# Kernel optimization log

Hardware: AMD Instinct MI355X
Metric: run time of the kernel (lower is better)

Reference implementation:

```python
import jax, jax.numpy as jnp
import numpy as np

N = 100000   # nodes
E = 1600000  # edges per meta-path graph
D_IN = 256
H = 4        # num_heads
F = 32       # out_feats per head
D_HID = H * F  # 128
D_SEM = 128  # semantic attention hidden dim
C = 8        # output classes
NEG_SLOPE = 0.2


def setup_inputs() -> dict:
    key = jax.random.key(0)
    ks = jax.random.split(key, 24)
    inp = {
        "x": jax.random.normal(ks[0], (N, D_IN), dtype=jnp.float32),
        "src0": jax.random.randint(ks[1], (E,), 0, N),
        "dst0": jax.random.randint(ks[2], (E,), 0, N),
        "ew0": jax.random.uniform(ks[3], (E,), dtype=jnp.float32),
        "src1": jax.random.randint(ks[4], (E,), 0, N),
        "dst1": jax.random.randint(ks[5], (E,), 0, N),
        "ew1": jax.random.uniform(ks[6], (E,), dtype=jnp.float32),
    }
    s_in = 1.0 / np.sqrt(D_IN)
    s_f = 1.0 / np.sqrt(F)
    s_h = 1.0 / np.sqrt(D_HID)
    s_s = 1.0 / np.sqrt(D_SEM)
    # GAT params for meta-path 0 and 1 (tuple feat -> separate fc_src/fc_dst)
    inp["Wsrc0"] = jax.random.normal(ks[7], (D_IN, D_HID), dtype=jnp.float32) * s_in
    inp["Wdst0"] = jax.random.normal(ks[8], (D_IN, D_HID), dtype=jnp.float32) * s_in
    inp["al0"] = jax.random.normal(ks[9], (H, F), dtype=jnp.float32) * s_f
    inp["ar0"] = jax.random.normal(ks[10], (H, F), dtype=jnp.float32) * s_f
    inp["b0"] = jnp.zeros((D_HID,), dtype=jnp.float32)
    inp["Wsrc1"] = jax.random.normal(ks[11], (D_IN, D_HID), dtype=jnp.float32) * s_in
    inp["Wdst1"] = jax.random.normal(ks[12], (D_IN, D_HID), dtype=jnp.float32) * s_in
    inp["al1"] = jax.random.normal(ks[13], (H, F), dtype=jnp.float32) * s_f
    inp["ar1"] = jax.random.normal(ks[14], (H, F), dtype=jnp.float32) * s_f
    inp["b1"] = jnp.zeros((D_HID,), dtype=jnp.float32)
    # Semantic attention: Linear(D_HID->128) -> tanh -> Linear(128->1, no bias)
    inp["Wp1"] = jax.random.normal(ks[15], (D_HID, D_SEM), dtype=jnp.float32) * s_h
    inp["bp1"] = jnp.zeros((D_SEM,), dtype=jnp.float32)
    inp["Wp2"] = jax.random.normal(ks[16], (D_SEM, 1), dtype=jnp.float32) * s_s
    # Prediction head
    inp["Wo"] = jax.random.normal(ks[17], (D_HID, C), dtype=jnp.float32) * s_h
    inp["bo"] = jnp.zeros((C,), dtype=jnp.float32)
    return inp


def gat_conv(x, Wsrc, Wdst, al, ar, b, src, dst, ew):
    # feat_src/feat_dst: [N, H, F]
    fs = (x @ Wsrc).reshape(N, H, F)
    fd = (x @ Wdst).reshape(N, H, F)
    el = jnp.einsum('nhf,hf->nh', fs, al)  # [N, H]
    er = jnp.einsum('nhf,hf->nh', fd, ar)  # [N, H]
    e = jax.nn.leaky_relu(el[src] + er[dst], negative_slope=NEG_SLOPE)  # [E, H]
    a = jax.nn.sigmoid(e) * ew[:, None]  # [E, H]  (sigmoid attention * edge_weight)
    m = fs[src] * a[:, :, None]  # [E, H, F]
    out = jax.ops.segment_sum(m, dst, num_segments=N)  # [N, H, F]
    out = out + b.reshape(1, H, F)
    return jax.nn.elu(out).reshape(N, H * F)


def semantic_attention(z, Wp1, bp1, Wp2):
    # z: [N, P, D_HID]
    w = jnp.tanh(z @ Wp1 + bp1) @ Wp2  # [N, P, 1]
    w = w.mean(axis=0)                  # [P, 1]
    beta = jax.nn.softmax(w, axis=0)    # softmax over meta-paths
    return (beta[None] * z).sum(axis=1)  # [N, D_HID]


def reference(x, src0, dst0, ew0, src1, dst1, ew1,
              Wsrc0, Wdst0, al0, ar0, b0,
              Wsrc1, Wdst1, al1, ar1, b1,
              Wp1, bp1, Wp2, Wo, bo):
    z0 = gat_conv(x, Wsrc0, Wdst0, al0, ar0, b0, src0, dst0, ew0)
    z1 = gat_conv(x, Wsrc1, Wdst1, al1, ar1, b1, src1, dst1, ew1)
    z = jnp.stack([z0, z1], axis=1)  # [N, 2, H*F]
    h = semantic_attention(z, Wp1, bp1, Wp2)  # [N, H*F]
    return h @ Wo + bo  # [N, C]
```

## Files before the change

kernel.cpp:

```cpp
#include <hip/hip_runtime.h>
#include <hip/hip_fp16.h>
#include <math.h>

#define N_NODES 100000
#define N_EDGES 1600000
#define D_IN    256
#define D_HID   128
#define NH      4
#define NF      32
#define D_SEM   128
#define NC      8
#define NEG_SLOPE 0.2f
#define BUCKET  64
#define BIN_SHIFT 9
#define BINS    196
#define BIN_CAP 9216
#define CHUNK   8192

typedef _Float16 half8 __attribute__((ext_vector_type(8)));
typedef float    floatx4 __attribute__((ext_vector_type(4)));

__global__ void prep_fold(const float* __restrict__ Ws0, const float* __restrict__ al0,
                          const float* __restrict__ Wd0, const float* __restrict__ ar0,
                          const float* __restrict__ Ws1, const float* __restrict__ al1,
                          const float* __restrict__ Wd1, const float* __restrict__ ar1,
                          float* __restrict__ WF) {
    int d = threadIdx.x;
    for (int p = 0; p < 2; ++p) {
        const float* Ws = p ? Ws1 : Ws0;
        const float* al = p ? al1 : al0;
        const float* Wd = p ? Wd1 : Wd0;
        const float* ar = p ? ar1 : ar0;
        for (int h = 0; h < NH; ++h) {
            float se = 0.f, sr = 0.f;
            for (int f = 0; f < NF; ++f) {
                se = fmaf(Ws[d*D_HID + h*NF + f], al[h*NF + f], se);
                sr = fmaf(Wd[d*D_HID + h*NF + f], ar[h*NF + f], sr);
            }
            WF[d*16 + p*8 + h]     = se;
            WF[d*16 + p*8 + 4 + h] = sr;
        }
    }
}

__global__ __launch_bounds__(256) void prep_tr(const float* __restrict__ Ws0,
                                               const float* __restrict__ Ws1,
                                               const float* __restrict__ Wp1,
                                               __half* __restrict__ WT0,
                                               __half* __restrict__ WT1,
                                               __half* __restrict__ WP1T) {
    int g = blockIdx.x * 256 + threadIdx.x;
    if (g < 32768) {
        int c = g >> 8, k = g & 255;
        WT0[g] = __float2half_rn(Ws0[k*D_HID + c]);
    } else if (g < 65536) {
        int g2 = g - 32768;
        int c = g2 >> 8, k = g2 & 255;
        WT1[g2] = __float2half_rn(Ws1[k*D_HID + c]);
    } else {
        int g2 = g - 65536;
        int c = g2 >> 7, k = g2 & 127;
        WP1T[g2] = __float2half_rn(Wp1[k*D_SEM + c]);
    }
}

__global__ __launch_bounds__(256) void er_el_kernel(const float* __restrict__ x,
                                                    const float* __restrict__ WF,
                                                    float* __restrict__ eler) {
    __shared__ float xs[16][260];
    __shared__ float wfs[4096];
    int tid = threadIdx.x;
    #pragma unroll
    for (int i = 0; i < 16; ++i) wfs[tid + i*256] = WF[tid + i*256];
    int n0 = blockIdx.x * 16;
    #pragma unroll
    for (int i = 0; i < 4; ++i) {
        int id = tid + i*256;
        int r = id >> 6, c = (id & 63) << 2;
        *(float4*)&xs[r][c] = *(const float4*)&x[(size_t)(n0 + r)*D_IN + c];
    }
    __syncthreads();
    int node = tid >> 4, c = tid & 15;
    float s = 0.f;
    #pragma unroll 8
    for (int k = 0; k < 256; ++k) s = fmaf(xs[node][k], wfs[k*16 + c], s);
    int p = c >> 3, e = (c >> 2) & 1, h = c & 3;
    eler[(p*2 + e)*400000 + (n0 + node)*4 + h] = s;
}

__global__ __launch_bounds__(256) void gemm_fs_mfma(const float* __restrict__ x,
                                                    const __half* __restrict__ WT,
                                                    __half* __restrict__ FS) {
    __shared__ unsigned short xs[64][64];
    __shared__ unsigned short ws[128][64];
    int tid = threadIdx.x;
    int row0 = blockIdx.x * 64;
    int wid = tid >> 6, lane = tid & 63;
    int wm = wid >> 1, wn = wid & 1;
    int lr = lane & 15, lk = lane >> 4;

    floatx4 acc[2][4];
    #pragma unroll
    for (int m = 0; m < 2; ++m)
        #pragma unroll
        for (int n = 0; n < 4; ++n) acc[m][n] = (floatx4){0.f, 0.f, 0.f, 0.f};

    for (int k0 = 0; k0 < D_IN; k0 += 64) {
        #pragma unroll
        for (int i = 0; i < 4; ++i) {
            int id = tid + i*256;
            int r = id >> 4, c4 = (id & 15) << 2;
            int grow = row0 + r;
            float4 v = make_float4(0.f, 0.f, 0.f, 0.f);
            if (grow < N_NODES) v = *(const float4*)&x[(size_t)grow*D_IN + k0 + c4];
            __half2 p0 = __floats2half2_rn(v.x, v.y);
            __half2 p1 = __floats2half2_rn(v.z, v.w);
            uint2 pk; pk.x = *(unsigned*)&p0; pk.y = *(unsigned*)&p1;
            int cc = (((c4 >> 3) ^ (r & 7)) << 3) + (c4 & 7);
            *(uint2*)&xs[r][cc] = pk;
        }
        #pragma unroll
        for (int i = 0; i < 8; ++i) {
            int id = tid + i*256;
            int col = id >> 4, c4 = (id & 15) << 2;
            uint2 pk = *(const uint2*)&WT[col*256 + k0 + c4];
            int cc = (((c4 >> 3) ^ (col & 7)) << 3) + (c4 & 7);
            *(uint2*)&ws[col][cc] = pk;
        }
        __syncthreads();
        #pragma unroll
        for (int kk = 0; kk < 2; ++kk) {
            int ksub = kk*4 + lk;
            half8 a[2], b[4];
            #pragma unroll
            for (int m = 0; m < 2; ++m) {
                int r = wm*32 + m*16 + lr;
                a[m] = *(half8*)&xs[r][((ksub ^ (r & 7)) << 3)];
            }
            #pragma unroll
            for (int n = 0; n < 4; ++n) {
                int c = wn*64 + n*16 + lr;
                b[n] = *(half8*)&ws[c][((ksub ^ (c & 7)) << 3)];
            }
            #pragma unroll
            for (int m = 0; m < 2; ++m)
                #pragma unroll
                for (int n = 0; n < 4; ++n)
                    acc[m][n] = __builtin_amdgcn_mfma_f32_16x16x32_f16(a[m], b[n], acc[m][n], 0, 0, 0);
        }
        __syncthreads();
    }

    unsigned short* outs = &ws[0][0];
    #pragma unroll
    for (int m = 0; m < 2; ++m)
        #pragma unroll
        for (int n = 0; n < 4; ++n) {
            int col = wn*64 + n*16 + lr;
            #pragma unroll
            for (int r4 = 0; r4 < 4; ++r4) {
                int rr = wm*32 + m*16 + lk*4 + r4;
                __half hv = __float2half_rn(acc[m][n][r4]);
                outs[rr*128 + col] = *(unsigned short*)&hv;
            }
        }
    __syncthreads();
    #pragma unroll
    for (int i = 0; i < 8; ++i) {
        int id = tid + i*256;
        int r = id >> 5, c4 = (id & 31) << 2;
        int grow = row0 + r;
        if (grow < N_NODES)
            *(uint2*)&FS[(size_t)grow*D_HID + c4] = *(uint2*)&outs[r*128 + c4];
    }
}

__global__ __launch_bounds__(1024) void bin_kernel(const int* __restrict__ src,
                                                   const int* __restrict__ dst,
                                                   const float* __restrict__ ew,
                                                   int* __restrict__ gcur,
                                                   uint2* __restrict__ binned) {
    __shared__ uint2 stage[CHUNK];
    __shared__ unsigned char binof[CHUNK];
    __shared__ int bcnt[256], boff[256], gbase[256], brun[256];
    int tid = threadIdx.x;
    int c0 = blockIdx.x * CHUNK;
    int C = N_EDGES - c0; if (C > CHUNK) C = CHUNK;
    if (C <= 0) return;

    if (tid < 256) bcnt[tid] = 0;
    __syncthreads();
    for (int j = tid; j < C; j += 1024)
        atomicAdd(&bcnt[dst[c0 + j] >> BIN_SHIFT], 1);
    __syncthreads();

    int v = (tid < 256) ? bcnt[tid] : 0;
    if (tid < 256) boff[tid] = v;
    __syncthreads();
    for (int o = 1; o < 256; o <<= 1) {
        int u = (tid < 256 && tid >= o) ? boff[tid - o] : 0;
        __syncthreads();
        if (tid < 256) boff[tid] += u;
        __syncthreads();
    }
    if (tid < 256) {
        boff[tid] -= v;
        brun[tid] = 0;
        if (tid < BINS) gbase[tid] = v ? atomicAdd(&gcur[tid], v) : 0;
    }
    __syncthreads();

    for (int j = tid; j < C; j += 1024) {
        int e = c0 + j;
        int d = dst[e];
        int b = d >> BIN_SHIFT;
        unsigned q = (unsigned)(ew[e] * 32767.f + 0.5f);
        int p = atomicAdd(&brun[b], 1);
        int sl = boff[b] + p;
        stage[sl] = make_uint2(((unsigned)src[e] << 15) | q, (unsigned)d);
        binof[sl] = (unsigned char)b;
    }
    __syncthreads();

    for (int j = tid; j < C; j += 1024) {
        int b = binof[j];
        int off = gbase[b] + (j - boff[b]);
        if (off < BIN_CAP) binned[b * BIN_CAP + off] = stage[j];
    }
}

__global__ __launch_bounds__(1024) void bucket_kernel(const int* __restrict__ gcur,
                                                      const uint2* __restrict__ binned,
                                                      int* __restrict__ cnt,
                                                      unsigned* __restrict__ edg) {
    __shared__ unsigned buck[512 * BUCKET];
    __shared__ int lcnt[512];
    int tid = threadIdx.x;
    int b = blockIdx.x;
    int n0 = b << BIN_SHIFT;
    if (tid < 512) lcnt[tid] = 0;
    __syncthreads();

    int cE = gcur[b]; if (cE > BIN_CAP) cE = BIN_CAP;
    for (int j = tid; j < cE; j += 1024) {
        uint2 r = binned[b * BIN_CAP + j];
        int dl = (int)r.y - n0;
        int p = atomicAdd(&lcnt[dl], 1);
        if (p < BUCKET) buck[(dl << 6) + p] = r.x;
    }
    __syncthreads();

    const uint4* b4 = (const uint4*)buck;
    uint4* e4 = (uint4*)edg;
    for (int i = tid; i < 512 * BUCKET / 4; i += 1024) {
        int node = n0 + (i >> 4);
        if (node < N_NODES) e4[((size_t)node << 4) + (i & 15)] = b4[i];
    }
    if (tid < 512) {
        int node = n0 + tid;
        if (node < N_NODES) cnt[node] = lcnt[tid] < BUCKET ? lcnt[tid] : BUCKET;
    }
}

__global__ __launch_bounds__(256) void agg_kernel(const __half* __restrict__ FS,
                                                  const float* __restrict__ el,
                                                  const float* __restrict__ er,
                                                  const int* __restrict__ cnt,
                                                  const unsigned* __restrict__ edg,
                                                  const float* __restrict__ bias,
                                                  float* __restrict__ z) {
    int wv = (blockIdx.x * 256 + threadIdx.x) >> 6;
    int lane = threadIdx.x & 63;
    if (wv >= N_NODES) return;
    int q  = lane >> 4;
    int ql = lane & 15;
    int h  = ql >> 2;
    float erh = er[wv*4 + h];
    int cn = cnt[wv];
    if (cn > BUCKET) cn = BUCKET;
    int beg = wv << 6;

    float4 a0 = make_float4(0.f,0.f,0.f,0.f);
    float4 a1 = make_float4(0.f,0.f,0.f,0.f);

    for (int j = q; j < cn; j += 4) {
        unsigned p = edg[beg + j];
        int s = p >> 15;
        float w = (float)(p & 32767u) * (1.f / 32767.f);
        float v = el[s*4 + h] + erh;
        v = v > 0.f ? v : NEG_SLOPE * v;
        float a = w / (1.f + __expf(-v));
        uint4 raw = *(const uint4*)&FS[s*D_HID + (ql << 3)];
        float2 f0 = __half22float2(*(__half2*)&raw.x);
        float2 f1 = __half22float2(*(__half2*)&raw.y);
        float2 f2 = __half22float2(*(__half2*)&raw.z);
        float2 f3 = __half22float2(*(__half2*)&raw.w);
        a0.x = fmaf(f0.x, a, a0.x); a0.y = fmaf(f0.y, a, a0.y);
        a0.z = fmaf(f1.x, a, a0.z); a0.w = fmaf(f1.y, a, a0.w);
        a1.x = fmaf(f2.x, a, a1.x); a1.y = fmaf(f2.y, a, a1.y);
        a1.z = fmaf(f3.x, a, a1.z); a1.w = fmaf(f3.y, a, a1.w);
    }

    #pragma unroll
    for (int o = 16; o < 64; o <<= 1) {
        a0.x += __shfl_xor(a0.x, o); a0.y += __shfl_xor(a0.y, o);
        a0.z += __shfl_xor(a0.z, o); a0.w += __shfl_xor(a0.w, o);
        a1.x += __shfl_xor(a1.x, o); a1.y += __shfl_xor(a1.y, o);
        a1.z += __shfl_xor(a1.z, o); a1.w += __shfl_xor(a1.w, o);
    }

    if (q < 2) {
        int c = (ql << 3) + (q << 2);
        float4 r = q ? a1 : a0;
        float4 bv = *(const float4*)&bias[c];
        r.x += bv.x; r.y += bv.y; r.z += bv.z; r.w += bv.w;
        r.x = r.x > 0.f ? r.x : expm1f(r.x);
        r.y = r.y > 0.f ? r.y : expm1f(r.y);
        r.z = r.z > 0.f ? r.z : expm1f(r.z);
        r.w = r.w > 0.f ? r.w : expm1f(r.w);
        *(float4*)&z[wv*D_HID + c] = r;
    }
}

__global__ __launch_bounds__(256) void sem_mfma(const float* __restrict__ z0,
                                                const float* __restrict__ z1,
                                                const __half* __restrict__ WP1T,
                                                const float* __restrict__ bp1,
                                                const float* __restrict__ Wp2,
                                                float* __restrict__ wsum) {
    __shared__ unsigned short zs[64][128];
    __shared__ unsigned short ps[128][128];
    __shared__ float red[4];
    const float* z = blockIdx.y ? z1 : z0;
    int tid = threadIdx.x;
    int row0 = blockIdx.x * 64;
    int wid = tid >> 6, lane = tid & 63;
    int wm = wid >> 1, wn = wid & 1;
    int lr = lane & 15, lk = lane >> 4;

    #pragma unroll
    for (int i = 0; i < 8; ++i) {
        int id = tid + i*256;
        int r = id >> 5, c4 = (id & 31) << 2;
        int grow = row0 + r;
        float4 v = make_float4(0.f, 0.f, 0.f, 0.f);
        if (grow < N_NODES) v = *(const float4*)&z[(size_t)grow*D_HID + c4];
        __half2 p0 = __floats2half2_rn(v.x, v.y);
        __half2 p1 = __floats2half2_rn(v.z, v.w);
        uint2 pk; pk.x = *(unsigned*)&p0; pk.y = *(unsigned*)&p1;
        int cc = (((c4 >> 3) ^ (r & 7)) << 3) + (c4 & 7);
        *(uint2*)&zs[r][cc] = pk;
    }
    #pragma unroll
    for (int i = 0; i < 16; ++i) {
        int id = tid + i*256;
        int c = id >> 5, k4 = (id & 31) << 2;
        uint2 pk = *(const uint2*)&WP1T[c*128 + k4];
        int cc = (((k4 >> 3) ^ (c & 7)) << 3) + (k4 & 7);
        *(uint2*)&ps[c][cc] = pk;
    }
    __syncthreads();

    floatx4 acc[2][4];
    #pragma unroll
    for (int m = 0; m < 2; ++m)
        #pragma unroll
        for (int n = 0; n < 4; ++n) acc[m][n] = (floatx4){0.f, 0.f, 0.f, 0.f};

    #pragma unroll
    for (int kk = 0; kk < 4; ++kk) {
        int ksub = kk*4 + lk;
        half8 a[2], b[4];
        #pragma unroll
        for (int m = 0; m < 2; ++m) {
            int r = wm*32 + m*16 + lr;
            a[m] = *(half8*)&zs[r][((ksub ^ (r & 7)) << 3)];
        }
        #pragma unroll
        for (int n = 0; n < 4; ++n) {
            int c = wn*64 + n*16 + lr;
            b[n] = *(half8*)&ps[c][((ksub ^ (c & 7)) << 3)];
        }
        #pragma unroll
        for (int m = 0; m < 2; ++m)
            #pragma unroll
            for (int n = 0; n < 4; ++n)
                acc[m][n] = __builtin_amdgcn_mfma_f32_16x16x32_f16(a[m], b[n], acc[m][n], 0, 0, 0);
    }

    float s = 0.f;
    #pragma unroll
    for (int m = 0; m < 2; ++m)
        #pragma unroll
        for (int n = 0; n < 4; ++n) {
            int col = wn*64 + n*16 + lr;
            float bp = bp1[col];
            float w2 = Wp2[col];
            #pragma unroll
            for (int r4 = 0; r4 < 4; ++r4) {
                int grow = row0 + wm*32 + m*16 + lk*4 + r4;
                if (grow < N_NODES) {
                    float v = acc[m][n][r4] + bp;
                    float t = 1.f - 2.f / (__expf(2.f*v) + 1.f);
                    s = fmaf(t, w2, s);
                }
            }
        }
    #pragma unroll
    for (int o = 1; o < 64; o <<= 1) s += __shfl_xor(s, o);
    if (lane == 0) red[wid] = s;
    __syncthreads();
    if (tid == 0) atomicAdd(&wsum[blockIdx.y], red[0] + red[1] + red[2] + red[3]);
}

__global__ __launch_bounds__(256) void final_kernel(const float* __restrict__ z0,
                                                    const float* __restrict__ z1,
                                                    const float* __restrict__ Wo,
                                                    const float* __restrict__ bo,
                                                    const float* __restrict__ wsum,
                                                    float* __restrict__ out) {
    __shared__ float z0s[32][132];
    __shared__ float z1s[32][132];
    __shared__ float wos[128*8];
    __shared__ float bos[8];
    int tid = threadIdx.x;
    int n0 = blockIdx.x * 32;
    #pragma unroll
    for (int i = 0; i < 4; ++i) wos[tid + i*256] = Wo[tid + i*256];
    if (tid < 8) bos[tid] = bo[tid];
    #pragma unroll
    for (int i = 0; i < 4; ++i) {
        int idx = tid + i*256;
        int r = idx >> 5, c = (idx & 31) << 2;
        *(float4*)&z0s[r][c] = *(const float4*)&z0[(n0 + r)*D_HID + c];
        *(float4*)&z1s[r][c] = *(const float4*)&z1[(n0 + r)*D_HID + c];
    }
    __syncthreads();

    float w0 = wsum[0] * (1.f / N_NODES), w1 = wsum[1] * (1.f / N_NODES);
    float m = fmaxf(w0, w1);
    float e0 = __expf(w0 - m), e1 = __expf(w1 - m);
    float b0 = e0 / (e0 + e1), b1 = 1.f - b0;

    int node = tid >> 3, c = tid & 7;
    float s = bos[c];
    #pragma unroll 8
    for (int k = 0; k < 128; ++k) {
        float hk = b0 * z0s[node][k] + b1 * z1s[node][k];
        s = fmaf(hk, wos[k*8 + c], s);
    }
    out[(n0 + node)*NC + c] = s;
}

extern "C" void kernel_launch(void* const* d_in, const int* in_sizes, int n_in,
                              void* d_out, int out_size, void* d_ws, size_t ws_size,
                              hipStream_t stream) {
    const float* x     = (const float*)d_in[0];
    const int*   src0  = (const int*)  d_in[1];
    const int*   dst0  = (const int*)  d_in[2];
    const float* ew0   = (const float*)d_in[3];
    const int*   src1  = (const int*)  d_in[4];
    const int*   dst1  = (const int*)  d_in[5];
    const float* ew1   = (const float*)d_in[6];
    const float* Wsrc0 = (const float*)d_in[7];
    const float* Wdst0 = (const float*)d_in[8];
    const float* al0   = (const float*)d_in[9];
    const float* ar0   = (const float*)d_in[10];
    const float* b0    = (const float*)d_in[11];
    const float* Wsrc1 = (const float*)d_in[12];
    const float* Wdst1 = (const float*)d_in[13];
    const float* al1   = (const float*)d_in[14];
    const float* ar1   = (const float*)d_in[15];
    const float* b1    = (const float*)d_in[16];
    const float* Wp1   = (const float*)d_in[17];
    const float* bp1   = (const float*)d_in[18];
    const float* Wp2   = (const float*)d_in[19];
    const float* Wo    = (const float*)d_in[20];
    const float* bo    = (const float*)d_in[21];
    float* out = (float*)d_out;

    float*    ws     = (float*)d_ws;
    __half*   FS     = (__half*)ws;
    float*    Z0     = ws    + 6400000;
    float*    Z1     = Z0    + 12800000;
    float*    ELER   = Z1    + 12800000;
    float*    WF     = ELER  + 1600000;
    float*    WSUM   = WF    + 4096;
    __half*   WT0    = (__half*)(WSUM + 8);
    __half*   WT1    = (__half*)((float*)WT0 + 16384);
    __half*   WP1T   = (__half*)((float*)WT1 + 16384);
    int*      CNT0   = (int*)((float*)WP1T + 8192);
    int*      CNT1   = CNT0  + 100000;
    int*      GCUR0  = CNT1  + 100000;
    int*      GCUR1  = GCUR0 + 256;
    unsigned* EDG    = (unsigned*)(GCUR1 + 256);
    uint2*    BINNED = (uint2*)(EDG + 6400000);

    hipMemsetAsync(GCUR0, 0, sizeof(int)*512, stream);
    hipMemsetAsync(WSUM, 0, sizeof(float)*4, stream);

    prep_fold<<<1, 256, 0, stream>>>(Wsrc0, al0, Wdst0, ar0, Wsrc1, al1, Wdst1, ar1, WF);
    prep_tr<<<320, 256, 0, stream>>>(Wsrc0, Wsrc1, Wp1, WT0, WT1, WP1T);
    er_el_kernel<<<N_NODES/16, 256, 0, stream>>>(x, WF, ELER);

    bin_kernel<<<BINS, 1024, 0, stream>>>(src0, dst0, ew0, GCUR0, BINNED);
    bucket_kernel<<<BINS, 1024, 0, stream>>>(GCUR0, BINNED, CNT0, EDG);
    gemm_fs_mfma<<<(N_NODES + 63)/64, 256, 0, stream>>>(x, WT0, FS);
    agg_kernel<<<(N_NODES*64)/256, 256, 0, stream>>>(FS, ELER, ELER + 400000, CNT0, EDG, b0, Z0);

    bin_kernel<<<BINS, 1024, 0, stream>>>(src1, dst1, ew1, GCUR1, BINNED);
    bucket_kernel<<<BINS, 1024, 0, stream>>>(GCUR1, BINNED, CNT1, EDG);
    gemm_fs_mfma<<<(N_NODES + 63)/64, 256, 0, stream>>>(x, WT1, FS);
    agg_kernel<<<(N_NODES*64)/256, 256, 0, stream>>>(FS, ELER + 800000, ELER + 1200000, CNT1, EDG, b1, Z1);

    dim3 semgrid((N_NODES + 63)/64, 2);
    sem_mfma<<<semgrid, 256, 0, stream>>>(Z0, Z1, WP1T, bp1, Wp2, WSUM);
    final_kernel<<<N_NODES/32, 256, 0, stream>>>(Z0, Z1, Wo, bo, WSUM, out);
}
```

Baseline: 640.3 us.

## Cache fp16 copy of x, skip unused bucket writes, unroll aggregation loop

The er/el kernel now also writes an fp16 copy of x into the Z1 buffer, which is free at that point. Both feature GEMMs read this half-precision copy, halving their input traffic and dropping the per-tile conversion. The bucket kernel writes only the edge-slot groups a node actually uses, and the aggregation loop is unrolled by two with a fast reciprocal so two gathers are in flight at once. The trade-off is an extra 51MB write in er_el and more registers in the aggregation kernel.

```diff
diff --git a/kernel.cpp b/kernel.cpp
--- a/kernel.cpp
+++ b/kernel.cpp
@@ -66,7 +66,8 @@
 
 __global__ __launch_bounds__(256) void er_el_kernel(const float* __restrict__ x,
                                                     const float* __restrict__ WF,
-                                                    float* __restrict__ eler) {
+                                                    float* __restrict__ eler,
+                                                    __half* __restrict__ XH) {
     __shared__ float xs[16][260];
     __shared__ float wfs[4096];
     int tid = threadIdx.x;
@@ -86,9 +87,20 @@
     for (int k = 0; k < 256; ++k) s = fmaf(xs[node][k], wfs[k*16 + c], s);
     int p = c >> 3, e = (c >> 2) & 1, h = c & 3;
     eler[(p*2 + e)*400000 + (n0 + node)*4 + h] = s;
-}
-
-__global__ __launch_bounds__(256) void gemm_fs_mfma(const float* __restrict__ x,
+
+    #pragma unroll
+    for (int i = 0; i < 4; ++i) {
+        int id = tid + i*256;
+        int r = id >> 6, c4 = (id & 63) << 2;
+        float4 v = *(const float4*)&xs[r][c4];
+        __half2 h0 = __floats2half2_rn(v.x, v.y);
+        __half2 h1 = __floats2half2_rn(v.z, v.w);
+        uint2 pk; pk.x = *(unsigned*)&h0; pk.y = *(unsigned*)&h1;
+        *(uint2*)&XH[(size_t)(n0 + r)*D_IN + c4] = pk;
+    }
+}
+
+__global__ __launch_bounds__(256) void gemm_fs_mfma(const __half* __restrict__ XH,
                                                     const __half* __restrict__ WT,
                                                     __half* __restrict__ FS) {
     __shared__ unsigned short xs[64][64];
@@ -107,17 +119,14 @@
 
     for (int k0 = 0; k0 < D_IN; k0 += 64) {
         #pragma unroll
-        for (int i = 0; i < 4; ++i) {
+        for (int i = 0; i < 2; ++i) {
             int id = tid + i*256;
-            int r = id >> 4, c4 = (id & 15) << 2;
+            int r = id >> 3, c8 = (id & 7) << 3;
             int grow = row0 + r;
-            float4 v = make_float4(0.f, 0.f, 0.f, 0.f);
-            if (grow < N_NODES) v = *(const float4*)&x[(size_t)grow*D_IN + k0 + c4];
-            __half2 p0 = __floats2half2_rn(v.x, v.y);
-            __half2 p1 = __floats2half2_rn(v.z, v.w);
-            uint2 pk; pk.x = *(unsigned*)&p0; pk.y = *(unsigned*)&p1;
-            int cc = (((c4 >> 3) ^ (r & 7)) << 3) + (c4 & 7);
-            *(uint2*)&xs[r][cc] = pk;
+            uint4 pk = make_uint4(0u, 0u, 0u, 0u);
+            if (grow < N_NODES) pk = *(const uint4*)&XH[(size_t)grow*D_IN + k0 + c8];
+            int cc = (((c8 >> 3) ^ (r & 7)) << 3);
+            *(uint4*)&xs[r][cc] = pk;
         }
         #pragma unroll
         for (int i = 0; i < 8; ++i) {
@@ -254,7 +263,9 @@
     uint4* e4 = (uint4*)edg;
     for (int i = tid; i < 512 * BUCKET / 4; i += 1024) {
         int node = n0 + (i >> 4);
-        if (node < N_NODES) e4[((size_t)node << 4) + (i & 15)] = b4[i];
+        int used = lcnt[i >> 4];
+        if (node < N_NODES && ((i & 15) << 2) < used)
+            e4[((size_t)node << 4) + (i & 15)] = b4[i];
     }
     if (tid < 512) {
         int node = n0 + tid;
@@ -279,18 +290,51 @@
     int cn = cnt[wv];
     if (cn > BUCKET) cn = BUCKET;
     int beg = wv << 6;
+    const __half* fsq = FS + (ql << 3);
 
     float4 a0 = make_float4(0.f,0.f,0.f,0.f);
     float4 a1 = make_float4(0.f,0.f,0.f,0.f);
 
-    for (int j = q; j < cn; j += 4) {
+    int j = q;
+    for (; j + 4 < cn; j += 8) {
+        unsigned p0 = edg[beg + j];
+        unsigned p1 = edg[beg + j + 4];
+        int s0 = p0 >> 15, s1 = p1 >> 15;
+        uint4 raw0 = *(const uint4*)&fsq[s0*D_HID];
+        uint4 raw1 = *(const uint4*)&fsq[s1*D_HID];
+        float v0 = el[s0*4 + h] + erh;
+        float v1 = el[s1*4 + h] + erh;
+        float w0 = (float)(p0 & 32767u) * (1.f / 32767.f);
+        float w1 = (float)(p1 & 32767u) * (1.f / 32767.f);
+        v0 = v0 > 0.f ? v0 : NEG_SLOPE * v0;
+        v1 = v1 > 0.f ? v1 : NEG_SLOPE * v1;
+        float ac0 = w0 * __builtin_amdgcn_rcpf(1.f + __expf(-v0));
+        float ac1 = w1 * __builtin_amdgcn_rcpf(1.f + __expf(-v1));
+        float2 f0 = __half22float2(*(__half2*)&raw0.x);
+        float2 f1 = __half22float2(*(__half2*)&raw0.y);
+        float2 f2 = __half22float2(*(__half2*)&raw0.z);
+        float2 f3 = __half22float2(*(__half2*)&raw0.w);
+        a0.x = fmaf(f0.x, ac0, a0.x); a0.y = fmaf(f0.y, ac0, a0.y);
+        a0.z = fmaf(f1.x, ac0, a0.z); a0.w = fmaf(f1.y, ac0, a0.w);
+        a1.x = fmaf(f2.x, ac0, a1.x); a1.y = fmaf(f2.y, ac0, a1.y);
+        a1.z = fmaf(f3.x, ac0, a1.z); a1.w = fmaf(f3.y, ac0, a1.w);
+        f0 = __half22float2(*(__half2*)&raw1.x);
+        f1 = __half22float2(*(__half2*)&raw1.y);
+        f2 = __half22float2(*(__half2*)&raw1.z);
+        f3 = __half22float2(*(__half2*)&raw1.w);
+        a0.x = fmaf(f0.x, ac1, a0.x); a0.y = fmaf(f0.y, ac1, a0.y);
+        a0.z = fmaf(f1.x, ac1, a0.z); a0.w = fmaf(f1.y, ac1, a0.w);
+        a1.x = fmaf(f2.x, ac1, a1.x); a1.y = fmaf(f2.y, ac1, a1.y);
+        a1.z = fmaf(f3.x, ac1, a1.z); a1.w = fmaf(f3.y, ac1, a1.w);
+    }
+    if (j < cn) {
         unsigned p = edg[beg + j];
         int s = p >> 15;
         float w = (float)(p & 32767u) * (1.f / 32767.f);
         float v = el[s*4 + h] + erh;
         v = v > 0.f ? v : NEG_SLOPE * v;
-        float a = w / (1.f + __expf(-v));
-        uint4 raw = *(const uint4*)&FS[s*D_HID + (ql << 3)];
+        float a = w * __builtin_amdgcn_rcpf(1.f + __expf(-v));
+        uint4 raw = *(const uint4*)&fsq[s*D_HID];
         float2 f0 = __half22float2(*(__half2*)&raw.x);
         float2 f1 = __half22float2(*(__half2*)&raw.y);
         float2 f2 = __half22float2(*(__half2*)&raw.z);
@@ -495,22 +539,23 @@
     int*      GCUR1  = GCUR0 + 256;
     unsigned* EDG    = (unsigned*)(GCUR1 + 256);
     uint2*    BINNED = (uint2*)(EDG + 6400000);
+    __half*   XH     = (__half*)Z1;
 
     hipMemsetAsync(GCUR0, 0, sizeof(int)*512, stream);
     hipMemsetAsync(WSUM, 0, sizeof(float)*4, stream);
 
     prep_fold<<<1, 256, 0, stream>>>(Wsrc0, al0, Wdst0, ar0, Wsrc1, al1, Wdst1, ar1, WF);
     prep_tr<<<320, 256, 0, stream>>>(Wsrc0, Wsrc1, Wp1, WT0, WT1, WP1T);
-    er_el_kernel<<<N_NODES/16, 256, 0, stream>>>(x, WF, ELER);
+    er_el_kernel<<<N_NODES/16, 256, 0, stream>>>(x, WF, ELER, XH);
 
     bin_kernel<<<BINS, 1024, 0, stream>>>(src0, dst0, ew0, GCUR0, BINNED);
     bucket_kernel<<<BINS, 1024, 0, stream>>>(GCUR0, BINNED, CNT0, EDG);
-    gemm_fs_mfma<<<(N_NODES + 63)/64, 256, 0, stream>>>(x, WT0, FS);
+    gemm_fs_mfma<<<(N_NODES + 63)/64, 256, 0, stream>>>(XH, WT0, FS);
     agg_kernel<<<(N_NODES*64)/256, 256, 0, stream>>>(FS, ELER, ELER + 400000, CNT0, EDG, b0, Z0);
 
     bin_kernel<<<BINS, 1024, 0, stream>>>(src1, dst1, ew1, GCUR1, BINNED);
     bucket_kernel<<<BINS, 1024, 0, stream>>>(GCUR1, BINNED, CNT1, EDG);
-    gemm_fs_mfma<<<(N_NODES + 63)/64, 256, 0, stream>>>(x, WT1, FS);
+    gemm_fs_mfma<<<(N_NODES + 63)/64, 256, 0, stream>>>(XH, WT1, FS);
     agg_kernel<<<(N_NODES*64)/256, 256, 0, stream>>>(FS, ELER + 800000, ELER + 1200000, CNT1, EDG, b1, Z1);
 
     dim3 semgrid((N_NODES + 63)/64, 2);
```

Result: faster. 616.9 us (-3.7%).
